# Kernel optimization log

Measured on AMD Instinct MI355X. Metric: run time of the kernel, lower is better.

## Reference

```python
import jax, jax.numpy as jnp
import numpy as np

B, N, D, H = 8, 1024, 512, 512  # batch, nodes/graph, input dim, hidden/output dim
NEG_SLOPE = 0.2


def _gatv2_layer(x, src, dst, Wl, bl, Wr, br, a, bias, nseg):
    """PyG GATv2Conv (heads=1, add_self_loops=False, eval mode -> no dropout).
    message j->i: alpha_ij = softmax_i( a . leaky_relu(xl[j] + xr[i]) ); out[i] = sum_j alpha_ij * xl[j] + bias
    """
    xl = x @ Wl + bl              # [nseg, H] source transform
    xr = x @ Wr + br              # [nseg, H] target transform
    e = jax.nn.leaky_relu(xl[src] + xr[dst], NEG_SLOPE) @ a  # [E] raw scores
    m = jax.lax.stop_gradient(jax.ops.segment_max(e, dst, num_segments=nseg))
    ex = jnp.exp(e - m[dst])
    s = jax.ops.segment_sum(ex, dst, num_segments=nseg)
    alpha = ex / s[dst]                                       # segment softmax over incoming edges
    out = jax.ops.segment_sum(alpha[:, None] * xl[src], dst, num_segments=nseg)
    return out + bias


def setup_inputs() -> dict:
    key = jax.random.key(0)
    rng = np.random.RandomState(0)
    # random per-graph adjacency, avg degree ~16; block-diagonal edge extraction
    adj_np = (rng.rand(B, N, N) < (16.0 / N))
    srcs, dsts = [], []
    for b in range(B):  # matches torch.nonzero(big_adj).t(): row=src, col=dst
        r, c = np.nonzero(adj_np[b])
        srcs.append(r + b * N)
        dsts.append(c + b * N)
    edge_index = jnp.asarray(np.stack([np.concatenate(srcs), np.concatenate(dsts)]).astype(np.int32))

    ks = jax.random.split(key, 32)
    def lin(k, fi, fo):
        return (jax.random.normal(k, (fi, fo), jnp.float32) / np.sqrt(fi)).astype(jnp.float32)
    inp = {
        "batch_graph": jax.random.normal(ks[0], (B, N, D), jnp.float32),
        "adj": jnp.asarray(adj_np.astype(np.float32)),
        "edge_index": edge_index,
    }
    dims = [(D, H), (H, H), (H, H)]
    for i, (fi, fo) in enumerate(dims, start=1):
        k = jax.random.split(ks[i], 6)
        inp[f"Wl{i}"] = lin(k[0], fi, fo)
        inp[f"bl{i}"] = jnp.zeros((fo,), jnp.float32)
        inp[f"Wr{i}"] = lin(k[1], fi, fo)
        inp[f"br{i}"] = jnp.zeros((fo,), jnp.float32)
        inp[f"a{i}"] = (jax.random.normal(k[2], (fo,), jnp.float32) / np.sqrt(fo)).astype(jnp.float32)
        inp[f"bias{i}"] = jnp.zeros((fo,), jnp.float32)
    return inp


def reference(batch_graph, adj, edge_index,
              Wl1, bl1, Wr1, br1, a1, bias1,
              Wl2, bl2, Wr2, br2, a2, bias2,
              Wl3, bl3, Wr3, br3, a3, bias3):
    b, n, d = batch_graph.shape
    nseg = b * n
    x = batch_graph.reshape(nseg, d)
    src, dst = edge_index[0], edge_index[1]
    x = _gatv2_layer(x, src, dst, Wl1, bl1, Wr1, br1, a1, bias1, nseg)  # graph_norm = Identity
    x = _gatv2_layer(x, src, dst, Wl2, bl2, Wr2, br2, a2, bias2, nseg)
    x = _gatv2_layer(x, src, dst, Wl3, bl3, Wr3, br3, a3, bias3, nseg)
    return x.reshape(b, n, -1)
```

## Files before the change

kernel.cpp:

```cpp
#include <hip/hip_runtime.h>
#include <math.h>

#define MTOT 8192
#define HD   512
#define NEG  0.2f
#define BPG  512

typedef __attribute__((ext_vector_type(8))) short bf16x8;
typedef __attribute__((ext_vector_type(4))) float floatx4;

__device__ inline unsigned short f2bf(float f) {
    unsigned int u = __float_as_uint(f);
    unsigned int r = (u + 0x7FFFu + ((u >> 16) & 1u)) >> 16;
    return (unsigned short)r;
}
__device__ inline float bf2f(unsigned short h) {
    return __uint_as_float(((unsigned int)h) << 16);
}


__global__ void zero_ints(int* p, int n) {
    int i = blockIdx.x * 256 + threadIdx.x;
    if (i < n) p[i] = 0;
}

__global__ void count_deg(const int* __restrict__ dst, int* __restrict__ deg, int E) {
    int i = blockIdx.x * 256 + threadIdx.x;
    if (i < E) atomicAdd(&deg[dst[i]], 1);
}

__global__ __launch_bounds__(1024) void scan_offsets(const int* __restrict__ deg,
                                                     int* __restrict__ offs,
                                                     int* __restrict__ cursor) {
    __shared__ int part[1024];
    int tid = threadIdx.x;
    int base = tid * 8;
    int v[8]; int s = 0;
    #pragma unroll
    for (int i = 0; i < 8; ++i) { v[i] = deg[base + i]; s += v[i]; }
    part[tid] = s;
    __syncthreads();
    for (int off = 1; off < 1024; off <<= 1) {
        int t = (tid >= off) ? part[tid - off] : 0;
        __syncthreads();
        part[tid] += t;
        __syncthreads();
    }
    int run = (tid == 0) ? 0 : part[tid - 1];
    #pragma unroll
    for (int i = 0; i < 8; ++i) {
        offs[base + i] = run;
        cursor[base + i] = run;
        run += v[i];
    }
    if (tid == 1023) offs[MTOT] = run;
}

__global__ void scatter_edges(const int* __restrict__ src, const int* __restrict__ dst,
                              int* __restrict__ cursor, int* __restrict__ csr_src,
                              int* __restrict__ csr_dst, int E) {
    int i = blockIdx.x * 256 + threadIdx.x;
    if (i < E) {
        int d = dst[i];
        int p = atomicAdd(&cursor[d], 1);
        csr_src[p] = src[i];
        csr_dst[p] = d;
    }
}


__global__ __launch_bounds__(256) void act_convert(const float* __restrict__ X,
                                                   unsigned short* __restrict__ Ahi,
                                                   unsigned short* __restrict__ Alo) {
    int i = (blockIdx.x * 256 + threadIdx.x) * 4;
    float4 v = *(const float4*)(X + i);
    ushort4 h, l;
    h.x = f2bf(v.x); l.x = f2bf(v.x - bf2f(h.x));
    h.y = f2bf(v.y); l.y = f2bf(v.y - bf2f(h.y));
    h.z = f2bf(v.z); l.z = f2bf(v.z - bf2f(h.z));
    h.w = f2bf(v.w); l.w = f2bf(v.w - bf2f(h.w));
    *(ushort4*)(Ahi + i) = h;
    *(ushort4*)(Alo + i) = l;
}

__global__ __launch_bounds__(256) void wt_convert_all(
    const float* __restrict__ W0, const float* __restrict__ W1,
    const float* __restrict__ W2, const float* __restrict__ W3,
    const float* __restrict__ W4, const float* __restrict__ W5,
    unsigned short* __restrict__ wtbase) {
    int z = blockIdx.z;
    const float* W = (z == 0) ? W0 : (z == 1) ? W1 : (z == 2) ? W2
                   : (z == 3) ? W3 : (z == 4) ? W4 : W5;
    int L = z >> 1, lr = z & 1;
    const size_t SZ = (size_t)HD * HD;
    unsigned short* Whi = wtbase + (L * 4 + lr * 2) * SZ;
    unsigned short* Wlo = Whi + SZ;

    __shared__ float t[32][33];
    int bx = blockIdx.x * 32;
    int by = blockIdx.y * 32;
    int tx = threadIdx.x & 31, ty = threadIdx.x >> 5;
    for (int i = ty; i < 32; i += 8)
        t[i][tx] = W[(size_t)(by + i) * HD + bx + tx];
    __syncthreads();
    for (int i = ty; i < 32; i += 8) {
        float v = t[tx][i];
        unsigned short h = f2bf(v);
        unsigned short l = f2bf(v - bf2f(h));
        Whi[(size_t)(bx + i) * HD + by + tx] = h;
        Wlo[(size_t)(bx + i) * HD + by + tx] = l;
    }
}


__global__ __launch_bounds__(256) void gemm_mfma_dual(
    const unsigned short* __restrict__ Ahi, const unsigned short* __restrict__ Alo,
    const unsigned short* __restrict__ Bhi_l, const unsigned short* __restrict__ Blo_l,
    const unsigned short* __restrict__ Bhi_r, const unsigned short* __restrict__ Blo_r,
    const float* __restrict__ bias_l, const float* __restrict__ bias_r,
    float* __restrict__ Cl, float* __restrict__ Cr)
{
    const unsigned short* Bhi = blockIdx.z ? Bhi_r : Bhi_l;
    const unsigned short* Blo = blockIdx.z ? Blo_r : Blo_l;
    const float* bias         = blockIdx.z ? bias_r : bias_l;
    float* C                  = blockIdx.z ? Cr : Cl;

    __shared__ __align__(16) unsigned short lds[4 * 128 * 32];

    int tid = threadIdx.x;
    int wave = tid >> 6, lane = tid & 63;
    int bm = blockIdx.y * 128, bn = blockIdx.x * 128;

    const unsigned short* gsrc[4] = {Ahi, Alo, Bhi, Blo};
    int rowbase[4] = {bm, bm, bn, bn};

    const unsigned short* gbase =
        gsrc[wave] + (size_t)(rowbase[wave] + (lane >> 2)) * 512 + (lane & 3) * 8;

    floatx4 acc[4][4] = {};

    int wm = wave & 1, wn = wave >> 1;
    int lr = lane & 15, lq = lane >> 4;

    for (int k0 = 0; k0 < 512; k0 += 32) {
        const unsigned short* g = gbase + k0;
        #pragma unroll
        for (int rg = 0; rg < 8; ++rg) {
            __builtin_amdgcn_global_load_lds(
                (const __attribute__((address_space(1))) unsigned int*)(g + (size_t)rg * 16 * 512),
                (__attribute__((address_space(3))) unsigned int*)(&lds[wave * 4096 + rg * 512]),
                16, 0, 0);
        }
        __syncthreads();

        bf16x8 ah[4], al[4], bh[4], bl_[4];
        #pragma unroll
        for (int i = 0; i < 4; ++i) {
            int mrow = wm * 64 + i * 16 + lr;
            ah[i]  = *(const bf16x8*)&lds[0 * 4096 + mrow * 32 + lq * 8];
            al[i]  = *(const bf16x8*)&lds[1 * 4096 + mrow * 32 + lq * 8];
            int nrow = wn * 64 + i * 16 + lr;
            bh[i]  = *(const bf16x8*)&lds[2 * 4096 + nrow * 32 + lq * 8];
            bl_[i] = *(const bf16x8*)&lds[3 * 4096 + nrow * 32 + lq * 8];
        }
        #pragma unroll
        for (int i = 0; i < 4; ++i)
            #pragma unroll
            for (int j = 0; j < 4; ++j) {
                acc[i][j] = __builtin_amdgcn_mfma_f32_16x16x32_bf16(ah[i], bh[j],  acc[i][j], 0, 0, 0);
                acc[i][j] = __builtin_amdgcn_mfma_f32_16x16x32_bf16(ah[i], bl_[j], acc[i][j], 0, 0, 0);
                acc[i][j] = __builtin_amdgcn_mfma_f32_16x16x32_bf16(al[i], bh[j],  acc[i][j], 0, 0, 0);
            }
        __syncthreads();
    }

    #pragma unroll
    for (int j = 0; j < 4; ++j) {
        int n = bn + wn * 64 + j * 16 + lr;
        float bv = bias[n];
        #pragma unroll
        for (int i = 0; i < 4; ++i) {
            int mbase = bm + wm * 64 + i * 16 + lq * 4;
            #pragma unroll
            for (int r = 0; r < 4; ++r)
                C[(size_t)(mbase + r) * 512 + n] = acc[i][j][r] + bv;
        }
    }
}


__global__ __launch_bounds__(256) void edge_scores(
    const float* __restrict__ xl, const float* __restrict__ xr,
    const float* __restrict__ avec,
    const int* __restrict__ offs, const int* __restrict__ csr_src,
    const int* __restrict__ csr_dst, float* __restrict__ escore)
{
    int g = blockIdx.x & 7;
    int chunk = blockIdx.x >> 3;
    int gb = offs[g << 10], ge = offs[(g + 1) << 10];
    int wave = threadIdx.x >> 6, lane = threadIdx.x & 63;
    int sub = lane >> 4, flane = lane & 15;

    float4 av[8];
    #pragma unroll
    for (int i = 0; i < 8; ++i)
        av[i] = *(const float4*)(avec + i * 64 + flane * 4);

    for (int base = gb + ((chunk << 2) + wave) * 4; base < ge; base += BPG * 16) {
        int p = base + sub;
        bool valid = p < ge;
        int srcn = valid ? csr_src[p] : 0;
        int dstn = valid ? csr_dst[p] : 0;
        const float* xls = xl + (size_t)srcn * HD;
        const float* xrs = xr + (size_t)dstn * HD;

        float pe = 0.f;
        #pragma unroll
        for (int i = 0; i < 8; ++i) {
            float4 xv = *(const float4*)(xls + i * 64 + flane * 4);
            float4 rv = *(const float4*)(xrs + i * 64 + flane * 4);
            float t;
            t = xv.x + rv.x; pe += av[i].x * (t > 0.f ? t : NEG * t);
            t = xv.y + rv.y; pe += av[i].y * (t > 0.f ? t : NEG * t);
            t = xv.z + rv.z; pe += av[i].z * (t > 0.f ? t : NEG * t);
            t = xv.w + rv.w; pe += av[i].w * (t > 0.f ? t : NEG * t);
        }
        pe += __shfl_xor(pe, 1, 64);
        pe += __shfl_xor(pe, 2, 64);
        pe += __shfl_xor(pe, 4, 64);
        pe += __shfl_xor(pe, 8, 64);
        if (valid && flane == 0) escore[p] = pe;
    }
}


__global__ __launch_bounds__(256) void gat_apply(
    const float* __restrict__ xl, const float* __restrict__ escore,
    const float* __restrict__ bias,
    const int* __restrict__ offs, const int* __restrict__ csr_src,
    float* __restrict__ out, unsigned short* __restrict__ Ohi,
    unsigned short* __restrict__ Olo, int write_fp32)
{
    __shared__ float alpha_sh[4][128];
    int gid = blockIdx.x;
    int node = ((gid & 7) << 10) + ((gid >> 3) << 2) + (threadIdx.x >> 6);
    int wv = threadIdx.x >> 6;
    int lane = threadIdx.x & 63;
    int h0 = lane << 2;

    int beg = offs[node], end = offs[node + 1];
    int deg = end - beg;
    if (deg > 128) deg = 128;

    float m = -1e30f;
    for (int i = lane; i < deg; i += 64) m = fmaxf(m, escore[beg + i]);
    #pragma unroll
    for (int off = 32; off; off >>= 1) m = fmaxf(m, __shfl_xor(m, off, 64));

    float s = 0.f;
    for (int i = lane; i < deg; i += 64) {
        float w = __expf(escore[beg + i] - m);
        alpha_sh[wv][i] = w;
        s += w;
    }
    #pragma unroll
    for (int off = 32; off; off >>= 1) s += __shfl_xor(s, off, 64);
    float inv = (s > 0.f) ? 1.f / s : 0.f;

    float4 acc0 = {0.f, 0.f, 0.f, 0.f}, acc1 = {0.f, 0.f, 0.f, 0.f};
    int p = 0;
    for (; p + 4 <= deg; p += 4) {
        float w0 = alpha_sh[wv][p + 0], w1 = alpha_sh[wv][p + 1];
        float w2 = alpha_sh[wv][p + 2], w3 = alpha_sh[wv][p + 3];
        int j0 = csr_src[beg + p + 0], j1 = csr_src[beg + p + 1];
        int j2 = csr_src[beg + p + 2], j3 = csr_src[beg + p + 3];
        const float* q0 = xl + (size_t)j0 * HD;
        const float* q1 = xl + (size_t)j1 * HD;
        const float* q2 = xl + (size_t)j2 * HD;
        const float* q3 = xl + (size_t)j3 * HD;
        float4 x00 = *(const float4*)(q0 + h0), x01 = *(const float4*)(q0 + 256 + h0);
        float4 x10 = *(const float4*)(q1 + h0), x11 = *(const float4*)(q1 + 256 + h0);
        float4 x20 = *(const float4*)(q2 + h0), x21 = *(const float4*)(q2 + 256 + h0);
        float4 x30 = *(const float4*)(q3 + h0), x31 = *(const float4*)(q3 + 256 + h0);
        acc0.x += w0 * x00.x + w1 * x10.x + w2 * x20.x + w3 * x30.x;
        acc0.y += w0 * x00.y + w1 * x10.y + w2 * x20.y + w3 * x30.y;
        acc0.z += w0 * x00.z + w1 * x10.z + w2 * x20.z + w3 * x30.z;
        acc0.w += w0 * x00.w + w1 * x10.w + w2 * x20.w + w3 * x30.w;
        acc1.x += w0 * x01.x + w1 * x11.x + w2 * x21.x + w3 * x31.x;
        acc1.y += w0 * x01.y + w1 * x11.y + w2 * x21.y + w3 * x31.y;
        acc1.z += w0 * x01.z + w1 * x11.z + w2 * x21.z + w3 * x31.z;
        acc1.w += w0 * x01.w + w1 * x11.w + w2 * x21.w + w3 * x31.w;
    }
    for (; p < deg; ++p) {
        float w = alpha_sh[wv][p];
        int j = csr_src[beg + p];
        const float* q = xl + (size_t)j * HD;
        float4 x0 = *(const float4*)(q + h0), x1 = *(const float4*)(q + 256 + h0);
        acc0.x += w * x0.x; acc0.y += w * x0.y; acc0.z += w * x0.z; acc0.w += w * x0.w;
        acc1.x += w * x1.x; acc1.y += w * x1.y; acc1.z += w * x1.z; acc1.w += w * x1.w;
    }

    float4 b0 = *(const float4*)(bias + h0);
    float4 b1 = *(const float4*)(bias + 256 + h0);
    float4 o0 = {acc0.x * inv + b0.x, acc0.y * inv + b0.y,
                 acc0.z * inv + b0.z, acc0.w * inv + b0.w};
    float4 o1 = {acc1.x * inv + b1.x, acc1.y * inv + b1.y,
                 acc1.z * inv + b1.z, acc1.w * inv + b1.w};

    if (write_fp32) {
        float* orow = out + (size_t)node * HD;
        *(float4*)(orow + h0) = o0;
        *(float4*)(orow + 256 + h0) = o1;
    } else {
        size_t rb = (size_t)node * HD;
        ushort4 h, lo;
        h.x = f2bf(o0.x); lo.x = f2bf(o0.x - bf2f(h.x));
        h.y = f2bf(o0.y); lo.y = f2bf(o0.y - bf2f(h.y));
        h.z = f2bf(o0.z); lo.z = f2bf(o0.z - bf2f(h.z));
        h.w = f2bf(o0.w); lo.w = f2bf(o0.w - bf2f(h.w));
        *(ushort4*)(Ohi + rb + h0) = h;
        *(ushort4*)(Olo + rb + h0) = lo;
        h.x = f2bf(o1.x); lo.x = f2bf(o1.x - bf2f(h.x));
        h.y = f2bf(o1.y); lo.y = f2bf(o1.y - bf2f(h.y));
        h.z = f2bf(o1.z); lo.z = f2bf(o1.z - bf2f(h.z));
        h.w = f2bf(o1.w); lo.w = f2bf(o1.w - bf2f(h.w));
        *(ushort4*)(Ohi + rb + 256 + h0) = h;
        *(ushort4*)(Olo + rb + 256 + h0) = lo;
    }
}


extern "C" void kernel_launch(void* const* d_in, const int* in_sizes, int n_in,
                              void* d_out, int out_size, void* d_ws, size_t ws_size,
                              hipStream_t stream) {
    const float* x0 = (const float*)d_in[0];
    const int* eidx = (const int*)d_in[2];
    int E = in_sizes[2] / 2;
    const int* esrc = eidx;
    const int* edst = eidx + E;

    const float* Wl[3] = {(const float*)d_in[3],  (const float*)d_in[9],  (const float*)d_in[15]};
    const float* bl[3] = {(const float*)d_in[4],  (const float*)d_in[10], (const float*)d_in[16]};
    const float* Wr[3] = {(const float*)d_in[5],  (const float*)d_in[11], (const float*)d_in[17]};
    const float* br[3] = {(const float*)d_in[6],  (const float*)d_in[12], (const float*)d_in[18]};
    const float* av[3] = {(const float*)d_in[7],  (const float*)d_in[13], (const float*)d_in[19]};
    const float* bs[3] = {(const float*)d_in[8],  (const float*)d_in[14], (const float*)d_in[20]};

    char* w = (char*)d_ws;
    unsigned short* Ahi = (unsigned short*)w; w += (size_t)MTOT * HD * 2;
    unsigned short* Alo = (unsigned short*)w; w += (size_t)MTOT * HD * 2;
    unsigned short* wtbase = (unsigned short*)w; w += 12 * (size_t)HD * HD * 2;
    float* xl = (float*)w; w += (size_t)MTOT * HD * 4;
    float* xr = (float*)w; w += (size_t)MTOT * HD * 4;
    float* escore = (float*)w; w += (size_t)E * 4;
    int* deg    = (int*)w;
    int* offs   = deg + MTOT;
    int* cursor = offs + MTOT + 8;
    int* csr    = cursor + MTOT;
    int* csrd   = csr + E;
    const size_t SZ = (size_t)HD * HD;

    dim3 wtg(16, 16, 6);
    wt_convert_all<<<wtg, 256, 0, stream>>>(Wl[0], Wr[0], Wl[1], Wr[1], Wl[2], Wr[2], wtbase);

    zero_ints<<<(MTOT + 255) / 256, 256, 0, stream>>>(deg, MTOT);
    count_deg<<<(E + 255) / 256, 256, 0, stream>>>(edst, deg, E);
    scan_offsets<<<1, 1024, 0, stream>>>(deg, offs, cursor);
    scatter_edges<<<(E + 255) / 256, 256, 0, stream>>>(esrc, edst, cursor, csr, csrd, E);

    act_convert<<<(MTOT * HD / 4 + 255) / 256, 256, 0, stream>>>(x0, Ahi, Alo);

    dim3 ggrid(HD / 128, MTOT / 128, 2);
    for (int L = 0; L < 3; ++L) {
        gemm_mfma_dual<<<ggrid, 256, 0, stream>>>(Ahi, Alo,
            wtbase + (L * 4 + 0) * SZ, wtbase + (L * 4 + 1) * SZ,
            wtbase + (L * 4 + 2) * SZ, wtbase + (L * 4 + 3) * SZ,
            bl[L], br[L], xl, xr);
        edge_scores<<<8 * BPG, 256, 0, stream>>>(xl, xr, av[L], offs, csr, csrd, escore);
        int last = (L == 2);
        gat_apply<<<MTOT / 4, 256, 0, stream>>>(xl, escore, bs[L], offs, csr,
                                                last ? (float*)d_out : nullptr,
                                                last ? nullptr : Ahi,
                                                last ? nullptr : Alo,
                                                last);
    }
}
```

Measured before the change: 368.9 us.

## Fuse edge scoring into per-node aggregation and merge setup kernels

Edge score computation now runs inside the per-destination-node softmax/aggregation kernel, so the xr row is loaded once per node and scores stay in shared memory instead of going through a global escore buffer. CSR construction is collapsed into one single-block kernel using shared-memory counters, and activation conversion is folded into the weight conversion launch, which cuts the number of launches. The single-block CSR build serialises E edges over 1024 threads, and the fused kernel reads xl rows for each neighbor in two passes per node.

```diff
diff --git a/kernel.cpp b/kernel.cpp
--- a/kernel.cpp
+++ b/kernel.cpp
@@ -4,7 +4,6 @@
 #define MTOT 8192
 #define HD   512
 #define NEG  0.2f
-#define BPG  512
 
 typedef __attribute__((ext_vector_type(8))) short bf16x8;
 typedef __attribute__((ext_vector_type(4))) float floatx4;
@@ -19,25 +18,24 @@
 }
 
 
-__global__ void zero_ints(int* p, int n) {
-    int i = blockIdx.x * 256 + threadIdx.x;
-    if (i < n) p[i] = 0;
-}
-
-__global__ void count_deg(const int* __restrict__ dst, int* __restrict__ deg, int E) {
-    int i = blockIdx.x * 256 + threadIdx.x;
-    if (i < E) atomicAdd(&deg[dst[i]], 1);
-}
-
-__global__ __launch_bounds__(1024) void scan_offsets(const int* __restrict__ deg,
-                                                     int* __restrict__ offs,
-                                                     int* __restrict__ cursor) {
+__global__ __launch_bounds__(1024) void csr_build(
+    const int* __restrict__ src, const int* __restrict__ dst, int E,
+    int* __restrict__ offs, int* __restrict__ csr_src)
+{
+    __shared__ int cnt[MTOT];
+    __shared__ int cur[MTOT];
     __shared__ int part[1024];
     int tid = threadIdx.x;
+
+    for (int i = tid; i < MTOT; i += 1024) cnt[i] = 0;
+    __syncthreads();
+    for (int i = tid; i < E; i += 1024) atomicAdd(&cnt[dst[i]], 1);
+    __syncthreads();
+
     int base = tid * 8;
     int v[8]; int s = 0;
     #pragma unroll
-    for (int i = 0; i < 8; ++i) { v[i] = deg[base + i]; s += v[i]; }
+    for (int i = 0; i < 8; ++i) { v[i] = cnt[base + i]; s += v[i]; }
     part[tid] = s;
     __syncthreads();
     for (int off = 1; off < 1024; off <<= 1) {
@@ -50,45 +48,46 @@
     #pragma unroll
     for (int i = 0; i < 8; ++i) {
         offs[base + i] = run;
-        cursor[base + i] = run;
+        cur[base + i] = run;
         run += v[i];
     }
     if (tid == 1023) offs[MTOT] = run;
-}
-
-__global__ void scatter_edges(const int* __restrict__ src, const int* __restrict__ dst,
-                              int* __restrict__ cursor, int* __restrict__ csr_src,
-                              int* __restrict__ csr_dst, int E) {
-    int i = blockIdx.x * 256 + threadIdx.x;
-    if (i < E) {
+    __syncthreads();
+
+    for (int i = tid; i < E; i += 1024) {
         int d = dst[i];
-        int p = atomicAdd(&cursor[d], 1);
+        int p = atomicAdd(&cur[d], 1);
         csr_src[p] = src[i];
-        csr_dst[p] = d;
-    }
-}
-
-
-__global__ __launch_bounds__(256) void act_convert(const float* __restrict__ X,
-                                                   unsigned short* __restrict__ Ahi,
-                                                   unsigned short* __restrict__ Alo) {
-    int i = (blockIdx.x * 256 + threadIdx.x) * 4;
-    float4 v = *(const float4*)(X + i);
-    ushort4 h, l;
-    h.x = f2bf(v.x); l.x = f2bf(v.x - bf2f(h.x));
-    h.y = f2bf(v.y); l.y = f2bf(v.y - bf2f(h.y));
-    h.z = f2bf(v.z); l.z = f2bf(v.z - bf2f(h.z));
-    h.w = f2bf(v.w); l.w = f2bf(v.w - bf2f(h.w));
-    *(ushort4*)(Ahi + i) = h;
-    *(ushort4*)(Alo + i) = l;
-}
-
-__global__ __launch_bounds__(256) void wt_convert_all(
+    }
+}
+
+
+__global__ __launch_bounds__(256) void prep_convert(
     const float* __restrict__ W0, const float* __restrict__ W1,
     const float* __restrict__ W2, const float* __restrict__ W3,
     const float* __restrict__ W4, const float* __restrict__ W5,
-    unsigned short* __restrict__ wtbase) {
+    unsigned short* __restrict__ wtbase,
+    const float* __restrict__ X,
+    unsigned short* __restrict__ Ahi, unsigned short* __restrict__ Alo)
+{
     int z = blockIdx.z;
+    if (z == 6) {
+        int bid = blockIdx.x * 16 + blockIdx.y;
+        int t0 = bid * 256 + threadIdx.x;
+        #pragma unroll
+        for (int it = 0; it < 16; ++it) {
+            int i = (t0 + it * 65536) * 4;
+            float4 vv = *(const float4*)(X + i);
+            ushort4 h, l;
+            h.x = f2bf(vv.x); l.x = f2bf(vv.x - bf2f(h.x));
+            h.y = f2bf(vv.y); l.y = f2bf(vv.y - bf2f(h.y));
+            h.z = f2bf(vv.z); l.z = f2bf(vv.z - bf2f(h.z));
+            h.w = f2bf(vv.w); l.w = f2bf(vv.w - bf2f(h.w));
+            *(ushort4*)(Ahi + i) = h;
+            *(ushort4*)(Alo + i) = l;
+        }
+        return;
+    }
     const float* W = (z == 0) ? W0 : (z == 1) ? W1 : (z == 2) ? W2
                    : (z == 3) ? W3 : (z == 4) ? W4 : W5;
     int L = z >> 1, lr = z & 1;
@@ -104,9 +103,9 @@
         t[i][tx] = W[(size_t)(by + i) * HD + bx + tx];
     __syncthreads();
     for (int i = ty; i < 32; i += 8) {
-        float v = t[tx][i];
-        unsigned short h = f2bf(v);
-        unsigned short l = f2bf(v - bf2f(h));
+        float vv = t[tx][i];
+        unsigned short h = f2bf(vv);
+        unsigned short l = f2bf(vv - bf2f(h));
         Whi[(size_t)(bx + i) * HD + by + tx] = h;
         Wlo[(size_t)(bx + i) * HD + by + tx] = l;
     }
@@ -189,89 +188,75 @@
 }
 
 
-__global__ __launch_bounds__(256) void edge_scores(
+__global__ __launch_bounds__(256) void gat_fused(
     const float* __restrict__ xl, const float* __restrict__ xr,
-    const float* __restrict__ avec,
-    const int* __restrict__ offs, const int* __restrict__ csr_src,
-    const int* __restrict__ csr_dst, float* __restrict__ escore)
-{
-    int g = blockIdx.x & 7;
-    int chunk = blockIdx.x >> 3;
-    int gb = offs[g << 10], ge = offs[(g + 1) << 10];
-    int wave = threadIdx.x >> 6, lane = threadIdx.x & 63;
-    int sub = lane >> 4, flane = lane & 15;
-
-    float4 av[8];
-    #pragma unroll
-    for (int i = 0; i < 8; ++i)
-        av[i] = *(const float4*)(avec + i * 64 + flane * 4);
-
-    for (int base = gb + ((chunk << 2) + wave) * 4; base < ge; base += BPG * 16) {
-        int p = base + sub;
-        bool valid = p < ge;
-        int srcn = valid ? csr_src[p] : 0;
-        int dstn = valid ? csr_dst[p] : 0;
-        const float* xls = xl + (size_t)srcn * HD;
-        const float* xrs = xr + (size_t)dstn * HD;
-
-        float pe = 0.f;
-        #pragma unroll
-        for (int i = 0; i < 8; ++i) {
-            float4 xv = *(const float4*)(xls + i * 64 + flane * 4);
-            float4 rv = *(const float4*)(xrs + i * 64 + flane * 4);
-            float t;
-            t = xv.x + rv.x; pe += av[i].x * (t > 0.f ? t : NEG * t);
-            t = xv.y + rv.y; pe += av[i].y * (t > 0.f ? t : NEG * t);
-            t = xv.z + rv.z; pe += av[i].z * (t > 0.f ? t : NEG * t);
-            t = xv.w + rv.w; pe += av[i].w * (t > 0.f ? t : NEG * t);
-        }
-        pe += __shfl_xor(pe, 1, 64);
-        pe += __shfl_xor(pe, 2, 64);
-        pe += __shfl_xor(pe, 4, 64);
-        pe += __shfl_xor(pe, 8, 64);
-        if (valid && flane == 0) escore[p] = pe;
-    }
-}
-
-
-__global__ __launch_bounds__(256) void gat_apply(
-    const float* __restrict__ xl, const float* __restrict__ escore,
-    const float* __restrict__ bias,
+    const float* __restrict__ avec, const float* __restrict__ bias,
     const int* __restrict__ offs, const int* __restrict__ csr_src,
     float* __restrict__ out, unsigned short* __restrict__ Ohi,
     unsigned short* __restrict__ Olo, int write_fp32)
 {
-    __shared__ float alpha_sh[4][128];
+    __shared__ float sc_sh[4][128];
     int gid = blockIdx.x;
-    int node = ((gid & 7) << 10) + ((gid >> 3) << 2) + (threadIdx.x >> 6);
     int wv = threadIdx.x >> 6;
+    int node = ((gid & 7) << 10) + ((gid >> 3) << 2) + wv;
     int lane = threadIdx.x & 63;
-    int h0 = lane << 2;
 
     int beg = offs[node], end = offs[node + 1];
     int deg = end - beg;
     if (deg > 128) deg = 128;
 
-    float m = -1e30f;
-    for (int i = lane; i < deg; i += 64) m = fmaxf(m, escore[beg + i]);
+    {
+        int sub = lane >> 4, flane = lane & 15;
+        float4 av[8], rv[8];
+        const float* xrrow = xr + (size_t)node * HD;
+        #pragma unroll
+        for (int i = 0; i < 8; ++i) {
+            av[i] = *(const float4*)(avec + i * 64 + flane * 4);
+            rv[i] = *(const float4*)(xrrow + i * 64 + flane * 4);
+        }
+        for (int p0 = 0; p0 < deg; p0 += 4) {
+            int p = p0 + sub;
+            bool valid = p < deg;
+            int j = csr_src[beg + (valid ? p : 0)];
+            const float* xls = xl + (size_t)j * HD;
+            float pe = 0.f;
+            #pragma unroll
+            for (int i = 0; i < 8; ++i) {
+                float4 xv = *(const float4*)(xls + i * 64 + flane * 4);
+                float t;
+                t = xv.x + rv[i].x; pe += av[i].x * (t > 0.f ? t : NEG * t);
+                t = xv.y + rv[i].y; pe += av[i].y * (t > 0.f ? t : NEG * t);
+                t = xv.z + rv[i].z; pe += av[i].z * (t > 0.f ? t : NEG * t);
+                t = xv.w + rv[i].w; pe += av[i].w * (t > 0.f ? t : NEG * t);
+            }
+            pe += __shfl_xor(pe, 1, 64);
+            pe += __shfl_xor(pe, 2, 64);
+            pe += __shfl_xor(pe, 4, 64);
+            pe += __shfl_xor(pe, 8, 64);
+            if (valid && flane == 0) sc_sh[wv][p] = pe;
+        }
+    }
+
+    float s0v = (lane < deg) ? sc_sh[wv][lane] : -1e30f;
+    float s1v = (lane + 64 < deg) ? sc_sh[wv][lane + 64] : -1e30f;
+    float m = fmaxf(s0v, s1v);
     #pragma unroll
     for (int off = 32; off; off >>= 1) m = fmaxf(m, __shfl_xor(m, off, 64));
-
-    float s = 0.f;
-    for (int i = lane; i < deg; i += 64) {
-        float w = __expf(escore[beg + i] - m);
-        alpha_sh[wv][i] = w;
-        s += w;
-    }
+    float e0 = (lane < deg) ? __expf(s0v - m) : 0.f;
+    float e1 = (lane + 64 < deg) ? __expf(s1v - m) : 0.f;
+    if (lane < deg) sc_sh[wv][lane] = e0;
+    if (lane + 64 < deg) sc_sh[wv][lane + 64] = e1;
+    float s = e0 + e1;
     #pragma unroll
     for (int off = 32; off; off >>= 1) s += __shfl_xor(s, off, 64);
     float inv = (s > 0.f) ? 1.f / s : 0.f;
 
+    int h0 = lane << 2;
     float4 acc0 = {0.f, 0.f, 0.f, 0.f}, acc1 = {0.f, 0.f, 0.f, 0.f};
     int p = 0;
     for (; p + 4 <= deg; p += 4) {
-        float w0 = alpha_sh[wv][p + 0], w1 = alpha_sh[wv][p + 1];
-        float w2 = alpha_sh[wv][p + 2], w3 = alpha_sh[wv][p + 3];
+        float w0 = sc_sh[wv][p + 0], w1 = sc_sh[wv][p + 1];
+        float w2 = sc_sh[wv][p + 2], w3 = sc_sh[wv][p + 3];
         int j0 = csr_src[beg + p + 0], j1 = csr_src[beg + p + 1];
         int j2 = csr_src[beg + p + 2], j3 = csr_src[beg + p + 3];
         const float* q0 = xl + (size_t)j0 * HD;
@@ -292,7 +277,7 @@
         acc1.w += w0 * x01.w + w1 * x11.w + w2 * x21.w + w3 * x31.w;
     }
     for (; p < deg; ++p) {
-        float w = alpha_sh[wv][p];
+        float w = sc_sh[wv][p];
         int j = csr_src[beg + p];
         const float* q = xl + (size_t)j * HD;
         float4 x0 = *(const float4*)(q + h0), x1 = *(const float4*)(q + 256 + h0);
@@ -352,23 +337,14 @@
     unsigned short* wtbase = (unsigned short*)w; w += 12 * (size_t)HD * HD * 2;
     float* xl = (float*)w; w += (size_t)MTOT * HD * 4;
     float* xr = (float*)w; w += (size_t)MTOT * HD * 4;
-    float* escore = (float*)w; w += (size_t)E * 4;
-    int* deg    = (int*)w;
-    int* offs   = deg + MTOT;
-    int* cursor = offs + MTOT + 8;
-    int* csr    = cursor + MTOT;
-    int* csrd   = csr + E;
+    int* offs = (int*)w;
+    int* csr  = offs + MTOT + 8;
     const size_t SZ = (size_t)HD * HD;
 
-    dim3 wtg(16, 16, 6);
-    wt_convert_all<<<wtg, 256, 0, stream>>>(Wl[0], Wr[0], Wl[1], Wr[1], Wl[2], Wr[2], wtbase);
-
-    zero_ints<<<(MTOT + 255) / 256, 256, 0, stream>>>(deg, MTOT);
-    count_deg<<<(E + 255) / 256, 256, 0, stream>>>(edst, deg, E);
-    scan_offsets<<<1, 1024, 0, stream>>>(deg, offs, cursor);
-    scatter_edges<<<(E + 255) / 256, 256, 0, stream>>>(esrc, edst, cursor, csr, csrd, E);
-
-    act_convert<<<(MTOT * HD / 4 + 255) / 256, 256, 0, stream>>>(x0, Ahi, Alo);
+    prep_convert<<<dim3(16, 16, 7), 256, 0, stream>>>(
+        Wl[0], Wr[0], Wl[1], Wr[1], Wl[2], Wr[2], wtbase, x0, Ahi, Alo);
+
+    csr_build<<<1, 1024, 0, stream>>>(esrc, edst, E, offs, csr);
 
     dim3 ggrid(HD / 128, MTOT / 128, 2);
     for (int L = 0; L < 3; ++L) {
@@ -376,9 +352,8 @@
             wtbase + (L * 4 + 0) * SZ, wtbase + (L * 4 + 1) * SZ,
             wtbase + (L * 4 + 2) * SZ, wtbase + (L * 4 + 3) * SZ,
             bl[L], br[L], xl, xr);
-        edge_scores<<<8 * BPG, 256, 0, stream>>>(xl, xr, av[L], offs, csr, csrd, escore);
         int last = (L == 2);
-        gat_apply<<<MTOT / 4, 256, 0, stream>>>(xl, escore, bs[L], offs, csr,
+        gat_fused<<<MTOT / 4, 256, 0, stream>>>(xl, xr, av[L], bs[L], offs, csr,
                                                 last ? (float*)d_out : nullptr,
                                                 last ? nullptr : Ahi,
                                                 last ? nullptr : Alo,
```

Measured after the change: 506.8 us. 1.37x slower.
